# Kernel optimization log

Measured on AMD Instinct MI355X. Metric: run time of the kernel, lower is better.

Reference implementation:

```python
import jax, jax.numpy as jnp
import numpy as np

NUM_CLASSES = 80
STRIDES = (8, 16, 32)
INPUT_SIZE = 640
DIST_THRESH_SQ = 64.0 * 64.0  # assignment uses euclidean dist < 64; compare squared


def make_anchors(input_size):
    pts = []
    for s in STRIDES:
        n = input_size // s
        yv, xv = np.meshgrid(np.arange(n), np.arange(n), indexing='ij')
        g = np.stack([xv, yv], -1).reshape(-1, 2).astype(np.float32) * s + s // 2
        pts.append(g)
    return jnp.asarray(np.concatenate(pts, 0))  # [A, 2]


def bce_logits(x, t):
    # BCEWithLogits, elementwise: -(t*log_sigmoid(x) + (1-t)*log_sigmoid(-x))
    return -(t * jax.nn.log_sigmoid(x) + (1.0 - t) * jax.nn.log_sigmoid(-x))


def iou_loss(pred_boxes, target_boxes):
    # pred: (cx, cy, log_w, log_h); target: (cx, cy, w, h) in pixels
    pc = pred_boxes[:, :2]
    ps = jnp.exp(pred_boxes[:, 2:4])
    p1 = pc - ps / 2.0
    p2 = pc + ps / 2.0
    t1 = target_boxes[:, :2] - target_boxes[:, 2:4] / 2.0
    t2 = target_boxes[:, :2] + target_boxes[:, 2:4] / 2.0
    i1 = jnp.maximum(p1, t1)
    i2 = jnp.minimum(p2, t2)
    inter = jnp.clip(i2[:, 0] - i1[:, 0], 0.0) * jnp.clip(i2[:, 1] - i1[:, 1], 0.0)
    pa = (p2[:, 0] - p1[:, 0]) * (p2[:, 1] - p1[:, 1])
    ta = (t2[:, 0] - t1[:, 0]) * (t2[:, 1] - t1[:, 1])
    union = pa + ta - inter
    return 1.0 - inter / (union + 1e-06)


def setup_inputs() -> dict:
    key = jax.random.key(0)
    k1, k2, k3, k4, k5 = jax.random.split(key, 5)
    B, M = 64, 50
    A = sum((INPUT_SIZE // s) ** 2 for s in STRIDES)  # 8400
    predictions = jax.random.normal(k1, (B, A, 5 + NUM_CLASSES), dtype=jnp.float32)
    cls = jax.random.randint(k2, (B, M), 0, NUM_CLASSES).astype(jnp.float32)
    valid = jax.random.uniform(k3, (B, M)) < 0.6
    cls = jnp.where(valid, cls, -1.0)
    centers = jax.random.uniform(k4, (B, M, 2), minval=0.05, maxval=0.95)
    wh = jax.random.uniform(k5, (B, M, 2), minval=0.02, maxval=0.3)
    targets = jnp.concatenate([cls[..., None], centers, wh], axis=-1).astype(jnp.float32)
    return {"predictions": predictions, "targets": targets, "input_size": 640}


def _per_image(pred, tgt, anchors, num_classes, input_size):
    # pred: [A, 5+C], tgt: [M, 5]
    valid = tgt[:, 0] >= 0.0                              # [M]
    gt_cls = tgt[:, 0].astype(jnp.int32)                  # [M]
    gt_boxes = tgt[:, 1:5] * input_size                   # [M, 4] pixels
    diff = gt_boxes[:, None, :2] - anchors[None, :, :]    # [M, A, 2]
    d2 = jnp.sum(diff * diff, axis=-1)                    # [M, A] squared dist
    d2 = jnp.where(valid[:, None], d2, jnp.inf)
    matched = jnp.argmin(d2, axis=0)                      # [A]
    min_d2 = jnp.min(d2, axis=0)                          # [A]
    pos = min_d2 < DIST_THRESH_SQ                         # [A]
    posf = pos.astype(pred.dtype)
    num_pos = posf.sum()

    obj_loss = bce_logits(pred[:, 4], posf).mean()

    cls_t = jax.nn.one_hot(gt_cls[matched], num_classes, dtype=pred.dtype)  # [A, C]
    cls_bce = bce_logits(pred[:, 5:], cls_t)                                # [A, C]
    denom = jnp.maximum(num_pos, 1.0)
    cls_loss = jnp.where(num_pos > 0,
                         (cls_bce * posf[:, None]).sum() / (denom * num_classes), 0.0)

    iou_l = iou_loss(pred[:, :4], gt_boxes[matched])      # [A]
    box_loss = jnp.where(num_pos > 0, (iou_l * posf).sum() / denom, 0.0)
    return obj_loss, cls_loss, box_loss, num_pos


def reference(predictions, targets, input_size):
    anchors = make_anchors(int(input_size))               # [A, 2]
    fsize = jnp.float32(input_size)
    obj, cls, box, npos = jax.vmap(
        lambda p, t: _per_image(p, t, anchors, NUM_CLASSES, fsize)
    )(predictions, targets)
    obj_loss = obj.sum()
    cls_loss = cls.sum()
    box_loss = box.sum()
    num_fg = npos.sum()
    total = 5.0 * box_loss + obj_loss + cls_loss
    return total, box_loss, obj_loss, cls_loss, num_fg
```

## Files before the change

### kernel.cpp

```cpp
#include <hip/hip_runtime.h>
#include <math.h>

#define NUM_CLASSES 80
#define MT 50
#define ATOT 8400
#define CH 85
#define EPI (ATOT * CH)
#define BLOCK 256
#define CHUNK 256
#define NBY 33

__device__ __forceinline__ float softplus_fast(float x) {
    return fmaxf(x, 0.0f) + __logf(1.0f + __expf(-fabsf(x)));
}

__global__ __launch_bounds__(BLOCK) void yolox_fused(
        const float* __restrict__ pred,
        const float* __restrict__ tgt,
        const int*   __restrict__ isz,
        float* __restrict__ acc) {
    const int b  = blockIdx.y;
    const int by = blockIdx.x;
    const int a0 = by * CHUNK;
    const int nanch = min(CHUNK, ATOT - a0);

    __shared__ float2 sxy[64];
    __shared__ float2 swh[64];
    __shared__ float  scls[64];
    __shared__ int    snv;
    __shared__ int    smask[CHUNK];

    if (threadIdx.x < 64) {
        const int m = threadIdx.x;
        const float fsize = (float)(*isz);
        float c = -1.0f, x = 0.f, y = 0.f, w = 0.f, h = 0.f;
        if (m < MT) {
            const float* tb = tgt + (size_t)b * MT * 5 + (size_t)m * 5;
            c = tb[0];
            x = tb[1] * fsize; y = tb[2] * fsize;
            w = tb[3] * fsize; h = tb[4] * fsize;
        }
        const bool valid = (m < MT) && (c >= 0.0f);
        const unsigned long long ballot = __ballot(valid);
        const int slot = __popcll(ballot & ((1ull << threadIdx.x) - 1ull));
        if (valid) {
            sxy[slot]  = make_float2(x, y);
            swh[slot]  = make_float2(w, h);
            scls[slot] = c;
        }
        if (m == 0) snv = (int)__popcll(ballot);
    }
    __syncthreads();
    const int nv = snv;

    float box_s = 0.f, np_s = 0.f;
    int myMask = -1;

    const int a = a0 + threadIdx.x;
    if (threadIdx.x < nanch) {
        float ax, ay;
        if (a < 6400)      { const int yy = a / 80;              const int xx = a - yy * 80;  ax = (float)(xx * 8  + 4);  ay = (float)(yy * 8  + 4); }
        else if (a < 8000) { const int i2 = a - 6400; const int yy = i2 / 40; const int xx = i2 - yy * 40; ax = (float)(xx * 16 + 8);  ay = (float)(yy * 16 + 8); }
        else               { const int i2 = a - 8000; const int yy = i2 / 20; const int xx = i2 - yy * 20; ax = (float)(xx * 32 + 16); ay = (float)(yy * 32 + 16); }

        float best = INFINITY;
        int bestm = 0;
        for (int m = 0; m < nv; ++m) {
            const float2 g = sxy[m];
            const float dx = g.x - ax, dy = g.y - ay;
            const float d2 = dx * dx + dy * dy;
            if (d2 < best) { best = d2; bestm = m; }
        }
        const bool pos = best < 4096.0f;
        myMask = pos ? (int)scls[bestm] : -1;

        if (pos) {
            np_s = 1.0f;
            const float* p = pred + ((size_t)b * ATOT + (size_t)a) * CH;
            const float pcx = p[0], pcy = p[1];
            const float pw = __expf(p[2]), ph = __expf(p[3]);
            const float2 g  = sxy[bestm];
            const float2 wh = swh[bestm];
            const float p1x = pcx - pw * 0.5f, p2x = pcx + pw * 0.5f;
            const float p1y = pcy - ph * 0.5f, p2y = pcy + ph * 0.5f;
            const float t1x = g.x - wh.x * 0.5f, t2x = g.x + wh.x * 0.5f;
            const float t1y = g.y - wh.y * 0.5f, t2y = g.y + wh.y * 0.5f;
            const float iw = fminf(p2x, t2x) - fmaxf(p1x, t1x);
            const float ih = fminf(p2y, t2y) - fmaxf(p1y, t1y);
            const float inter = fmaxf(iw, 0.f) * fmaxf(ih, 0.f);
            const float pa = (p2x - p1x) * (p2y - p1y);
            const float ta = (t2x - t1x) * (t2y - t1y);
            const float uni = pa + ta - inter;
            box_s = 1.0f - inter / (uni + 1e-6f);
        }
    }
    smask[threadIdx.x] = myMask;
    __syncthreads();

    const float* pblock = pred + (size_t)b * EPI + (size_t)a0 * CH;
    const int NG = (nanch * CH) >> 2;

    float obj_s = 0.f, cls_s = 0.f;

    int gi = threadIdx.x;
    for (; gi + 3 * BLOCK < NG; gi += 4 * BLOCK) {
        int   ok[4], c0k[4], mk[4];
        bool  need[4];
        #pragma unroll
        for (int k = 0; k < 4; ++k) {
            const int o = (gi + k * BLOCK) << 2;
            const unsigned la = __umulhi((unsigned)o, 3233857729u) >> 6;
            ok[k]  = o;
            c0k[k] = o - (int)la * CH;
            mk[k]  = smask[la];
            need[k] = (c0k[k] >= 1 && c0k[k] <= 4) || (mk[k] >= 0 && c0k[k] >= 2);
        }
        float4 x[4];
        #pragma unroll
        for (int k = 0; k < 4; ++k) {
            x[k] = need[k] ? *(const float4*)(pblock + ok[k])
                           : make_float4(0.f, 0.f, 0.f, 0.f);
        }
        #pragma unroll
        for (int k = 0; k < 4; ++k) {
            if (!need[k]) continue;
            const int c0 = c0k[k];
            const int m  = mk[k];
            const bool mpos = m >= 0;
            const float xs[4] = {x[k].x, x[k].y, x[k].z, x[k].w};
            #pragma unroll
            for (int j = 0; j < 4; ++j) {
                const int c = c0 + j;
                const float xv = xs[j];
                if (c == 4) {
                    obj_s += softplus_fast(xv) - (mpos ? xv : 0.0f);
                } else if (c >= 5 && c < CH && mpos) {
                    cls_s += softplus_fast(xv) - ((c - 5 == m) ? xv : 0.0f);
                }
            }
        }
    }
    for (; gi < NG; gi += BLOCK) {
        const int o = gi << 2;
        const unsigned la = __umulhi((unsigned)o, 3233857729u) >> 6;
        const int c0 = o - (int)la * CH;
        const int m  = smask[la];
        const bool need1 = (c0 >= 1 && c0 <= 4) || (m >= 0 && c0 >= 2);
        if (!need1) continue;
        const float4 x = *(const float4*)(pblock + o);
        const bool mpos = m >= 0;
        const float xs[4] = {x.x, x.y, x.z, x.w};
        #pragma unroll
        for (int j = 0; j < 4; ++j) {
            const int c = c0 + j;
            const float xv = xs[j];
            if (c == 4) {
                obj_s += softplus_fast(xv) - (mpos ? xv : 0.0f);
            } else if (c >= 5 && c < CH && mpos) {
                cls_s += softplus_fast(xv) - ((c - 5 == m) ? xv : 0.0f);
            }
        }
    }

    float v0 = box_s, v1 = np_s, v2 = obj_s, v3 = cls_s;
    for (int off = 32; off > 0; off >>= 1) {
        v0 += __shfl_down(v0, off, 64);
        v1 += __shfl_down(v1, off, 64);
        v2 += __shfl_down(v2, off, 64);
        v3 += __shfl_down(v3, off, 64);
    }
    __shared__ float sred[BLOCK / 64][4];
    const int wave = threadIdx.x >> 6;
    const int lane = threadIdx.x & 63;
    if (lane == 0) {
        sred[wave][0] = v0; sred[wave][1] = v1;
        sred[wave][2] = v2; sred[wave][3] = v3;
    }
    __syncthreads();
    if (threadIdx.x == 0) {
        float t0 = 0.f, t1 = 0.f, t2 = 0.f, t3 = 0.f;
        #pragma unroll
        for (int w = 0; w < BLOCK / 64; ++w) {
            t0 += sred[w][0]; t1 += sred[w][1];
            t2 += sred[w][2]; t3 += sred[w][3];
        }
        float* slot = acc + ((size_t)b * NBY + by) * 4;
        slot[0] = t0; slot[1] = t1; slot[2] = t2; slot[3] = t3;
    }
}

__global__ __launch_bounds__(BLOCK) void yolox_stage2(
        const float* __restrict__ acc,
        float* __restrict__ out, int B) {
    float obj = 0.f, cls = 0.f, box = 0.f, np = 0.f;
    for (int bb = threadIdx.x; bb < B; bb += BLOCK) {
        float bs = 0.f, ps = 0.f, os = 0.f, cs = 0.f;
        const float* s = acc + (size_t)bb * NBY * 4;
        #pragma unroll
        for (int j = 0; j < NBY; ++j) {
            bs += s[j * 4 + 0]; ps += s[j * 4 + 1];
            os += s[j * 4 + 2]; cs += s[j * 4 + 3];
        }
        obj += os * (1.0f / (float)ATOT);
        const float denom = fmaxf(ps, 1.0f);
        cls += (ps > 0.f) ? cs / (denom * (float)NUM_CLASSES) : 0.f;
        box += (ps > 0.f) ? bs / denom : 0.f;
        np  += ps;
    }
    float v0 = obj, v1 = cls, v2 = box, v3 = np;
    for (int off = 32; off > 0; off >>= 1) {
        v0 += __shfl_down(v0, off, 64);
        v1 += __shfl_down(v1, off, 64);
        v2 += __shfl_down(v2, off, 64);
        v3 += __shfl_down(v3, off, 64);
    }
    __shared__ float sred[BLOCK / 64][4];
    const int wave = threadIdx.x >> 6;
    const int lane = threadIdx.x & 63;
    if (lane == 0) {
        sred[wave][0] = v0; sred[wave][1] = v1;
        sred[wave][2] = v2; sred[wave][3] = v3;
    }
    __syncthreads();
    if (threadIdx.x == 0) {
        float t0 = 0.f, t1 = 0.f, t2 = 0.f, t3 = 0.f;
        #pragma unroll
        for (int w = 0; w < BLOCK / 64; ++w) {
            t0 += sred[w][0]; t1 += sred[w][1];
            t2 += sred[w][2]; t3 += sred[w][3];
        }
        out[0] = 5.0f * t2 + t0 + t1;
        out[1] = t2;
        out[2] = t0;
        out[3] = t1;
        out[4] = t3;
    }
}

extern "C" void kernel_launch(void* const* d_in, const int* in_sizes, int n_in,
                              void* d_out, int out_size, void* d_ws, size_t ws_size,
                              hipStream_t stream) {
    const float* pred = (const float*)d_in[0];
    const float* tgt  = (const float*)d_in[1];
    const int*   isz  = (const int*)d_in[2];
    float* out = (float*)d_out;

    const int B = in_sizes[1] / (MT * 5);

    float* acc = (float*)d_ws;

    dim3 grid(NBY, B);
    yolox_fused<<<grid, BLOCK, 0, stream>>>(pred, tgt, isz, acc);

    yolox_stage2<<<1, BLOCK, 0, stream>>>(acc, out, B);
}
```

Before: 268.7 us.

## Compact positive anchors into a list and iterate only their class logits

```diff
diff --git a/kernel.cpp b/kernel.cpp
--- a/kernel.cpp
+++ b/kernel.cpp
@@ -9,6 +9,7 @@
 #define BLOCK 256
 #define CHUNK 256
 #define NBY 33
+#define NWAVE (BLOCK / 64)
 
 __device__ __forceinline__ float softplus_fast(float x) {
     return fmaxf(x, 0.0f) + __logf(1.0f + __expf(-fabsf(x)));
@@ -23,15 +24,17 @@
     const int by = blockIdx.x;
     const int a0 = by * CHUNK;
     const int nanch = min(CHUNK, ATOT - a0);
+    const int tid = threadIdx.x;
 
     __shared__ float2 sxy[64];
     __shared__ float2 swh[64];
     __shared__ float  scls[64];
     __shared__ int    snv;
-    __shared__ int    smask[CHUNK];
-
-    if (threadIdx.x < 64) {
-        const int m = threadIdx.x;
+    __shared__ int    swcnt[NWAVE];
+    __shared__ int    splist[CHUNK];
+
+    if (tid < 64) {
+        const int m = tid;
         const float fsize = (float)(*isz);
         float c = -1.0f, x = 0.f, y = 0.f, w = 0.f, h = 0.f;
         if (m < MT) {
@@ -42,7 +45,7 @@
         }
         const bool valid = (m < MT) && (c >= 0.0f);
         const unsigned long long ballot = __ballot(valid);
-        const int slot = __popcll(ballot & ((1ull << threadIdx.x) - 1ull));
+        const int slot = __popcll(ballot & ((1ull << tid) - 1ull));
         if (valid) {
             sxy[slot]  = make_float2(x, y);
             swh[slot]  = make_float2(w, h);
@@ -53,11 +56,13 @@
     __syncthreads();
     const int nv = snv;
 
-    float box_s = 0.f, np_s = 0.f;
-    int myMask = -1;
-
-    const int a = a0 + threadIdx.x;
-    if (threadIdx.x < nanch) {
+    const float* pblock = pred + (size_t)b * EPI + (size_t)a0 * CH;
+
+    float box_s = 0.f, np_s = 0.f, obj_s = 0.f;
+    int myCls = -1;
+
+    if (tid < nanch) {
+        const int a = a0 + tid;
         float ax, ay;
         if (a < 6400)      { const int yy = a / 80;              const int xx = a - yy * 80;  ax = (float)(xx * 8  + 4);  ay = (float)(yy * 8  + 4); }
         else if (a < 8000) { const int i2 = a - 6400; const int yy = i2 / 40; const int xx = i2 - yy * 40; ax = (float)(xx * 16 + 8);  ay = (float)(yy * 16 + 8); }
@@ -72,11 +77,14 @@
             if (d2 < best) { best = d2; bestm = m; }
         }
         const bool pos = best < 4096.0f;
-        myMask = pos ? (int)scls[bestm] : -1;
+
+        const float* p = pblock + tid * CH;
+        const float xo = p[4];
+        obj_s = softplus_fast(xo) - (pos ? xo : 0.0f);
 
         if (pos) {
-            np_s = 1.0f;
-            const float* p = pred + ((size_t)b * ATOT + (size_t)a) * CH;
+            myCls = (int)scls[bestm];
+            np_s  = 1.0f;
             const float pcx = p[0], pcy = p[1];
             const float pw = __expf(p[2]), ph = __expf(p[3]);
             const float2 g  = sxy[bestm];
@@ -94,93 +102,78 @@
             box_s = 1.0f - inter / (uni + 1e-6f);
         }
     }
-    smask[threadIdx.x] = myMask;
-    __syncthreads();
-
-    const float* pblock = pred + (size_t)b * EPI + (size_t)a0 * CH;
-    const int NG = (nanch * CH) >> 2;
-
-    float obj_s = 0.f, cls_s = 0.f;
-
-    int gi = threadIdx.x;
-    for (; gi + 3 * BLOCK < NG; gi += 4 * BLOCK) {
-        int   ok[4], c0k[4], mk[4];
-        bool  need[4];
+
+    const bool isPos = (myCls >= 0);
+    const unsigned long long bal = __ballot(isPos);
+    const int wave = tid >> 6;
+    const int lane = tid & 63;
+    if (lane == 0) swcnt[wave] = (int)__popcll(bal);
+    __syncthreads();
+    int woff = 0, npos = 0;
+    #pragma unroll
+    for (int w = 0; w < NWAVE; ++w) {
+        const int c = swcnt[w];
+        if (w < wave) woff += c;
+        npos += c;
+    }
+    if (isPos) {
+        const int slot = woff + (int)__popcll(bal & ((1ull << lane) - 1ull));
+        splist[slot] = (myCls << 8) | tid;
+    }
+    __syncthreads();
+
+    float cls_s = 0.f;
+    const int total = npos * NUM_CLASSES;
+
+    int i = tid;
+    for (; i + 3 * BLOCK < total; i += 4 * BLOCK) {
+        int   off[4], cc[4], mm[4];
         #pragma unroll
         for (int k = 0; k < 4; ++k) {
-            const int o = (gi + k * BLOCK) << 2;
-            const unsigned la = __umulhi((unsigned)o, 3233857729u) >> 6;
-            ok[k]  = o;
-            c0k[k] = o - (int)la * CH;
-            mk[k]  = smask[la];
-            need[k] = (c0k[k] >= 1 && c0k[k] <= 4) || (mk[k] >= 0 && c0k[k] >= 2);
-        }
-        float4 x[4];
-        #pragma unroll
-        for (int k = 0; k < 4; ++k) {
-            x[k] = need[k] ? *(const float4*)(pblock + ok[k])
-                           : make_float4(0.f, 0.f, 0.f, 0.f);
-        }
-        #pragma unroll
-        for (int k = 0; k < 4; ++k) {
-            if (!need[k]) continue;
-            const int c0 = c0k[k];
-            const int m  = mk[k];
-            const bool mpos = m >= 0;
-            const float xs[4] = {x[k].x, x[k].y, x[k].z, x[k].w};
-            #pragma unroll
-            for (int j = 0; j < 4; ++j) {
-                const int c = c0 + j;
-                const float xv = xs[j];
-                if (c == 4) {
-                    obj_s += softplus_fast(xv) - (mpos ? xv : 0.0f);
-                } else if (c >= 5 && c < CH && mpos) {
-                    cls_s += softplus_fast(xv) - ((c - 5 == m) ? xv : 0.0f);
-                }
-            }
-        }
-    }
-    for (; gi < NG; gi += BLOCK) {
-        const int o = gi << 2;
-        const unsigned la = __umulhi((unsigned)o, 3233857729u) >> 6;
-        const int c0 = o - (int)la * CH;
-        const int m  = smask[la];
-        const bool need1 = (c0 >= 1 && c0 <= 4) || (m >= 0 && c0 >= 2);
-        if (!need1) continue;
-        const float4 x = *(const float4*)(pblock + o);
-        const bool mpos = m >= 0;
-        const float xs[4] = {x.x, x.y, x.z, x.w};
-        #pragma unroll
-        for (int j = 0; j < 4; ++j) {
-            const int c = c0 + j;
-            const float xv = xs[j];
-            if (c == 4) {
-                obj_s += softplus_fast(xv) - (mpos ? xv : 0.0f);
-            } else if (c >= 5 && c < CH && mpos) {
-                cls_s += softplus_fast(xv) - ((c - 5 == m) ? xv : 0.0f);
-            }
-        }
+            const unsigned ii = (unsigned)(i + k * BLOCK);
+            const unsigned pi = ii / NUM_CLASSES;
+            const int c  = (int)(ii - pi * NUM_CLASSES);
+            const int pk = splist[pi];
+            const int a  = pk & 0xFF;
+            cc[k]  = c;
+            mm[k]  = pk >> 8;
+            off[k] = a * CH + 5 + c;
+        }
+        float x[4];
+        #pragma unroll
+        for (int k = 0; k < 4; ++k) x[k] = pblock[off[k]];
+        #pragma unroll
+        for (int k = 0; k < 4; ++k)
+            cls_s += softplus_fast(x[k]) - ((cc[k] == mm[k]) ? x[k] : 0.0f);
+    }
+    for (; i < total; i += BLOCK) {
+        const unsigned ii = (unsigned)i;
+        const unsigned pi = ii / NUM_CLASSES;
+        const int c  = (int)(ii - pi * NUM_CLASSES);
+        const int pk = splist[pi];
+        const int a  = pk & 0xFF;
+        const int m  = pk >> 8;
+        const float x = pblock[a * CH + 5 + c];
+        cls_s += softplus_fast(x) - ((c == m) ? x : 0.0f);
     }
 
     float v0 = box_s, v1 = np_s, v2 = obj_s, v3 = cls_s;
-    for (int off = 32; off > 0; off >>= 1) {
-        v0 += __shfl_down(v0, off, 64);
-        v1 += __shfl_down(v1, off, 64);
-        v2 += __shfl_down(v2, off, 64);
-        v3 += __shfl_down(v3, off, 64);
-    }
-    __shared__ float sred[BLOCK / 64][4];
-    const int wave = threadIdx.x >> 6;
-    const int lane = threadIdx.x & 63;
+    for (int off2 = 32; off2 > 0; off2 >>= 1) {
+        v0 += __shfl_down(v0, off2, 64);
+        v1 += __shfl_down(v1, off2, 64);
+        v2 += __shfl_down(v2, off2, 64);
+        v3 += __shfl_down(v3, off2, 64);
+    }
+    __shared__ float sred[NWAVE][4];
     if (lane == 0) {
         sred[wave][0] = v0; sred[wave][1] = v1;
         sred[wave][2] = v2; sred[wave][3] = v3;
     }
     __syncthreads();
-    if (threadIdx.x == 0) {
+    if (tid == 0) {
         float t0 = 0.f, t1 = 0.f, t2 = 0.f, t3 = 0.f;
         #pragma unroll
-        for (int w = 0; w < BLOCK / 64; ++w) {
+        for (int w = 0; w < NWAVE; ++w) {
             t0 += sred[w][0]; t1 += sred[w][1];
             t2 += sred[w][2]; t3 += sred[w][3];
         }
```

Measured after the change: 261.4 us, median of 2. -2.7%, faster.
